# Performance work log

Measured on AMD Instinct MI355X. Metric: run time of the kernel, lower is better.

Reference implementation:

```python
import jax, jax.numpy as jnp
import numpy as np

DT = 0.01
NJ = 7  # panda: 7 revolute joints, serial chain, fixed base
G_ACC = 9.81


def skew(v):
    x, y, z = v[..., 0], v[..., 1], v[..., 2]
    O = jnp.zeros_like(x)
    return jnp.stack([jnp.stack([O, -z, y], -1),
                      jnp.stack([z, O, -x], -1),
                      jnp.stack([-y, x, O], -1)], -2)


def rodrigues(axis, q):
    # axis [3], q [B] -> [B,3,3]
    K = skew(axis)
    K2 = K @ K
    s = jnp.sin(q)[:, None, None]
    c = jnp.cos(q)[:, None, None]
    return jnp.eye(3, dtype=q.dtype) + s * K + (1.0 - c) * K2


def xmot(E, r, v):
    # motion transform child<-parent; E [B,3,3], r [3], v [B,6] ([w;u] ordering)
    w, u = v[:, :3], v[:, 3:]
    wn = jnp.einsum('bij,bj->bi', E, w)
    un = jnp.einsum('bij,bj->bi', E, u - jnp.cross(jnp.broadcast_to(r, u.shape), w))
    return jnp.concatenate([wn, un], -1)


def crm(v, m):
    # motion cross product v x m
    w, u = v[:, :3], v[:, 3:]
    return jnp.concatenate([jnp.cross(w, m[:, :3]),
                            jnp.cross(w, m[:, 3:]) + jnp.cross(u, m[:, :3])], -1)


def crf(v, f):
    # force cross product v x* f
    w, u = v[:, :3], v[:, 3:]
    n, ff = f[:, :3], f[:, 3:]
    return jnp.concatenate([jnp.cross(w, n) + jnp.cross(u, ff), jnp.cross(w, ff)], -1)


def spatial_inertia(mass, com, inertia):
    # [NJ] / [NJ,3] / [NJ,3,3] -> [NJ,6,6] in [w;v] ordering
    cx = skew(com)
    m = mass[:, None, None]
    top = jnp.concatenate([inertia + m * (cx @ jnp.swapaxes(cx, -1, -2)), m * cx], -1)
    bot = jnp.concatenate([m * jnp.swapaxes(cx, -1, -2),
                           m * jnp.broadcast_to(jnp.eye(3, dtype=mass.dtype), cx.shape)], -1)
    return jnp.concatenate([top, bot], -2)


def aba(q, qd, tau, axes, R_fix, p_fix, mass, com, inertia):
    B = q.shape[0]
    I6 = spatial_inertia(mass, com, inertia)  # [NJ,6,6]
    E_l, S_l, v_l, c_l, IA_l, pA_l = [], [], [], [], [], []
    v_prev = None
    # pass 1: kinematics + bias terms
    for i in range(NJ):
        Rw = jnp.einsum('ij,bjk->bik', R_fix[i], rodrigues(axes[i], q[:, i]))
        E = jnp.swapaxes(Rw, -1, -2)  # parent->child rotation
        S = jnp.concatenate([axes[i], jnp.zeros(3, dtype=q.dtype)])  # [6]
        vJ = qd[:, i:i + 1] * S
        v_i = vJ if i == 0 else xmot(E, p_fix[i], v_prev) + vJ
        c_i = crm(v_i, vJ)
        Iv = jnp.einsum('ij,bj->bi', I6[i], v_i)
        pA_i = crf(v_i, Iv)
        E_l.append(E); S_l.append(S); v_l.append(v_i); c_l.append(c_i)
        IA_l.append(jnp.broadcast_to(I6[i], (B, 6, 6)))
        pA_l.append(pA_i)
        v_prev = v_i
    # pass 2: articulated inertia backward sweep
    U_l = [None] * NJ; d_l = [None] * NJ; uu_l = [None] * NJ
    for i in reversed(range(NJ)):
        S = S_l[i]; IA = IA_l[i]
        U = jnp.einsum('bij,j->bi', IA, S)
        d = jnp.einsum('bi,i->b', U, S)
        uu = tau[:, i] - jnp.einsum('bi,i->b', pA_l[i], S)
        U_l[i], d_l[i], uu_l[i] = U, d, uu
        if i > 0:
            Ia = IA - U[:, :, None] * U[:, None, :] / d[:, None, None]
            pa = pA_l[i] + jnp.einsum('bij,bj->bi', Ia, c_l[i]) + U * (uu / d)[:, None]
            E = E_l[i]; rX = skew(p_fix[i])
            Z = jnp.zeros_like(E)
            Xm = jnp.concatenate([jnp.concatenate([E, Z], -1),
                                  jnp.concatenate([-jnp.einsum('bij,jk->bik', E, rX), E], -1)], -2)
            IA_l[i - 1] = IA_l[i - 1] + jnp.einsum('bji,bjk,bkl->bil', Xm, Ia, Xm)
            fE = jnp.einsum('bji,bj->bi', E, pa[:, 3:])
            nP = jnp.einsum('bji,bj->bi', E, pa[:, :3]) + jnp.cross(jnp.broadcast_to(p_fix[i], fE.shape), fE)
            pA_l[i - 1] = pA_l[i - 1] + jnp.concatenate([nP, fE], -1)
    # pass 3: accelerations (base spatial accel = -gravity)
    a_prev = jnp.broadcast_to(jnp.array([0, 0, 0, 0, 0, G_ACC], dtype=q.dtype), (B, 6))
    qdd = []
    for i in range(NJ):
        ap = xmot(E_l[i], p_fix[i], a_prev) + c_l[i]
        qdd_i = (uu_l[i] - jnp.einsum('bi,bi->b', U_l[i], ap)) / d_l[i]
        a_prev = ap + qdd_i[:, None] * S_l[i]
        qdd.append(qdd_i)
    return jnp.stack(qdd, -1)  # [B,NJ]


def _rx(a):
    c, s = np.cos(a), np.sin(a)
    return np.array([[1, 0, 0], [0, c, -s], [0, s, c]], np.float32)


def setup_inputs() -> dict:
    key = jax.random.key(0)
    k1, k2 = jax.random.split(key)
    B = 262144
    x = 0.5 * jax.random.normal(k1, (B, 2 * NJ), dtype=jnp.float32)
    u = 5.0 * jax.random.normal(k2, (B, NJ), dtype=jnp.float32)
    angles = [0.0, -np.pi / 2, np.pi / 2, np.pi / 2, -np.pi / 2, np.pi / 2, np.pi / 2]
    R_fix = jnp.asarray(np.stack([_rx(a) for a in angles]).astype(np.float32))
    p_fix = jnp.asarray(np.array([[0, 0, 0.333], [0, 0, 0], [0, -0.316, 0], [0.0825, 0, 0],
                                  [-0.0825, 0.384, 0], [0, 0, 0], [0.088, 0, 0]], np.float32))
    axes = jnp.asarray(np.tile(np.array([0, 0, 1], np.float32), (NJ, 1)))
    mass = jnp.asarray(np.array([4.97, 0.65, 3.23, 3.59, 1.23, 1.67, 0.735], np.float32))
    com = jnp.asarray(np.array([[0.003, 0.002, -0.06], [-0.003, -0.028, 0.003], [0.027, 0.039, -0.066],
                                [-0.053, 0.104, 0.027], [-0.012, 0.041, -0.038], [0.06, -0.014, -0.011],
                                [0.01, -0.004, 0.061]], np.float32))
    diags = np.array([[0.7, 0.7, 0.01], [0.008, 0.028, 0.025], [0.037, 0.036, 0.011],
                      [0.026, 0.028, 0.031], [0.036, 0.036, 0.011], [0.002, 0.004, 0.005],
                      [0.012, 0.010, 0.005]], np.float32)
    inertia = jnp.asarray(np.stack([np.diag(v) for v in diags]).astype(np.float32))
    return {"x": x, "u": u, "axes": axes, "R_fix": R_fix, "p_fix": p_fix,
            "mass": mass, "com": com, "inertia": inertia}


def reference(x, u, axes, R_fix, p_fix, mass, com, inertia):
    q, v = x[:, :NJ], x[:, NJ:]
    a = aba(q, v, u, axes, R_fix, p_fix, mass, com, inertia)
    v_next = v + DT * a            # semi-implicit Euler
    q_next = q + DT * v_next
    return jnp.concatenate([q_next, v_next], -1)
```

## Files before the change

kernel.cpp:

```cpp
#include <hip/hip_runtime.h>

#define NJ 7
#define TB 256
static constexpr float DT_C    = 0.01f;
static constexpr float G_ACC_C = 9.81f;

static constexpr float RF[NJ][9] = {
    {1,0,0,  0,1,0,  0,0,1},
    {1,0,0,  0,0,1,  0,-1,0},
    {1,0,0,  0,0,-1, 0,1,0},
    {1,0,0,  0,0,-1, 0,1,0},
    {1,0,0,  0,0,1,  0,-1,0},
    {1,0,0,  0,0,-1, 0,1,0},
    {1,0,0,  0,0,-1, 0,1,0},
};
static constexpr float PFX[NJ][3] = {
    {0.f, 0.f, 0.333f},
    {0.f, 0.f, 0.f},
    {0.f, -0.316f, 0.f},
    {0.0825f, 0.f, 0.f},
    {-0.0825f, 0.384f, 0.f},
    {0.f, 0.f, 0.f},
    {0.088f, 0.f, 0.f},
};
static constexpr float MS[NJ] = {4.97f, 0.65f, 3.23f, 3.59f, 1.23f, 1.67f, 0.735f};
static constexpr float CM[NJ][3] = {
    {0.003f, 0.002f, -0.06f},
    {-0.003f, -0.028f, 0.003f},
    {0.027f, 0.039f, -0.066f},
    {-0.053f, 0.104f, 0.027f},
    {-0.012f, 0.041f, -0.038f},
    {0.06f, -0.014f, -0.011f},
    {0.01f, -0.004f, 0.061f},
};
static constexpr float ID[NJ][3] = {
    {0.7f, 0.7f, 0.01f},
    {0.008f, 0.028f, 0.025f},
    {0.037f, 0.036f, 0.011f},
    {0.026f, 0.028f, 0.031f},
    {0.036f, 0.036f, 0.011f},
    {0.002f, 0.004f, 0.005f},
    {0.012f, 0.01f, 0.005f},
};

#define MAKE_E(Rf, s, c)                                                     \
    float E00 = (Rf)[0]*(c) + (Rf)[1]*(s);                                   \
    float E01 = (Rf)[3]*(c) + (Rf)[4]*(s);                                   \
    float E02 = (Rf)[6]*(c) + (Rf)[7]*(s);                                   \
    float E10 = (Rf)[1]*(c) - (Rf)[0]*(s);                                   \
    float E11 = (Rf)[4]*(c) - (Rf)[3]*(s);                                   \
    float E12 = (Rf)[7]*(c) - (Rf)[6]*(s);                                   \
    float E20 = (Rf)[2];                                                     \
    float E21 = (Rf)[5];                                                     \
    float E22 = (Rf)[8];

extern "C" __global__ __launch_bounds__(256)
void aba_step_kernel(const float* __restrict__ x, const float* __restrict__ u,
                     float* __restrict__ out, int B)
{
    __shared__ float xbuf [TB * 14];
    __shared__ float ubuf [TB * 7];
    __shared__ float scbuf[TB * 14];

    const int tid = threadIdx.x;
    const int b0  = blockIdx.x * TB;
    const int nb  = min(TB, B - b0);

    if (nb == TB) {
        const float4* xv = (const float4*)(x + b0 * 14);
        float4*       xl = (float4*)xbuf;
        #pragma unroll
        for (int k = 0; k < 4; ++k) {
            int idx = tid + k * TB;
            if (idx < 896) xl[idx] = xv[idx];
        }
        const float4* uv = (const float4*)(u + b0 * 7);
        float4*       ul = (float4*)ubuf;
        #pragma unroll
        for (int k = 0; k < 2; ++k) {
            int idx = tid + k * TB;
            if (idx < 448) ul[idx] = uv[idx];
        }
    } else {
        int nx = nb * 14;
        for (int t = tid; t < nx; t += TB) xbuf[t] = x[b0 * 14 + t];
        int nu = nb * 7;
        for (int t = tid; t < nu; t += TB) ubuf[t] = u[b0 * 7 + t];
    }
    __syncthreads();

    if (tid < nb) {
        const float* xr  = xbuf  + tid * 14;
        const float* ur  = ubuf  + tid * 7;
        float*       scr = scbuf + tid * 14;

        float cl0[NJ], cl1[NJ], cl3[NJ], cl4[NJ];
        float pA[NJ][6];

        {
            float v0=0.f, v1=0.f, v2=0.f, v3=0.f, v4=0.f, v5=0.f;
            #pragma unroll
            for (int i = 0; i < NJ; ++i) {
                float qi = xr[i];
                float qd = xr[7 + i];
                float s, c;
                __sincosf(qi, &s, &c);
                scr[i]     = s;
                scr[7 + i] = c;
                MAKE_E(RF[i], s, c)
                if (i == 0) {
                    v0 = 0.f; v1 = 0.f; v2 = qd; v3 = 0.f; v4 = 0.f; v5 = 0.f;
                } else {
                    const float px = PFX[i][0], py = PFX[i][1], pz = PFX[i][2];
                    float t0 = v3 - (py*v2 - pz*v1);
                    float t1 = v4 - (pz*v0 - px*v2);
                    float t2 = v5 - (px*v1 - py*v0);
                    float nw0 = E00*v0 + E01*v1 + E02*v2;
                    float nw1 = E10*v0 + E11*v1 + E12*v2;
                    float nw2 = E20*v0 + E21*v1 + E22*v2;
                    float nu0 = E00*t0 + E01*t1 + E02*t2;
                    float nu1 = E10*t0 + E11*t1 + E12*t2;
                    float nu2 = E20*t0 + E21*t1 + E22*t2;
                    v0 = nw0; v1 = nw1; v2 = nw2 + qd;
                    v3 = nu0; v4 = nu1; v5 = nu2;
                }
                cl0[i] =  v1*qd;
                cl1[i] = -v0*qd;
                cl3[i] =  v4*qd;
                cl4[i] = -v3*qd;
                const float m  = MS[i];
                const float cx = CM[i][0], cy = CM[i][1], cz = CM[i][2];
                const float cc = cx*cx + cy*cy + cz*cz;
                const float A0 = ID[i][0] + m*(cc - cx*cx);
                const float A1 = -(m*cx*cy);
                const float A2 = -(m*cx*cz);
                const float A3 = ID[i][1] + m*(cc - cy*cy);
                const float A4 = -(m*cy*cz);
                const float A5 = ID[i][2] + m*(cc - cz*cz);
                float n0 = A0*v0 + A1*v1 + A2*v2 + m*(cy*v5 - cz*v4);
                float n1 = A1*v0 + A3*v1 + A4*v2 + m*(cz*v3 - cx*v5);
                float n2 = A2*v0 + A4*v1 + A5*v2 + m*(cx*v4 - cy*v3);
                float f0 = m*(v1*cz - v2*cy + v3);
                float f1 = m*(v2*cx - v0*cz + v4);
                float f2 = m*(v0*cy - v1*cx + v5);
                pA[i][0] = v1*n2 - v2*n1 + v4*f2 - v5*f1;
                pA[i][1] = v2*n0 - v0*n2 + v5*f0 - v3*f2;
                pA[i][2] = v0*n1 - v1*n0 + v3*f1 - v4*f0;
                pA[i][3] = v1*f2 - v2*f1;
                pA[i][4] = v2*f0 - v0*f2;
                pA[i][5] = v0*f1 - v1*f0;
            }
        }

        float PA[6] = {0,0,0,0,0,0};
        float PB[9] = {0,0,0,0,0,0,0,0,0};
        float PC[6] = {0,0,0,0,0,0};

        #pragma unroll
        for (int ii = 0; ii < NJ; ++ii) {
            const int i = NJ - 1 - ii;
            const float m  = MS[i];
            const float cx = CM[i][0], cy = CM[i][1], cz = CM[i][2];
            const float cc = cx*cx + cy*cy + cz*cz;
            float A0 = ID[i][0] + m*(cc - cx*cx) + PA[0];
            float A1 = -(m*cx*cy)               + PA[1];
            float A2 = -(m*cx*cz)               + PA[2];
            float A3 = ID[i][1] + m*(cc - cy*cy) + PA[3];
            float A4 = -(m*cy*cz)               + PA[4];
            float A5 = ID[i][2] + m*(cc - cz*cz) + PA[5];
            float B00 = PB[0];          float B01 = PB[1] - m*cz;  float B02 = PB[2] + m*cy;
            float B10 = PB[3] + m*cz;   float B11 = PB[4];         float B12 = PB[5] - m*cx;
            float B20 = PB[6] - m*cy;   float B21 = PB[7] + m*cx;  float B22 = PB[8];
            float C0 = PC[0] + m, C1 = PC[1],     C2 = PC[2];
            float C3 = PC[3] + m, C4 = PC[4],     C5 = PC[5] + m;

            float uu   = ur[i] - pA[i][2];
            float invd = __builtin_amdgcn_rcpf(A5);
            float k    = uu * invd;
            float t0 = A2*invd, t1 = A4*invd;
            float t3 = B20*invd, t4 = B21*invd, t5 = B22*invd;

            if (i > 0) {
                float a00 = A0 - A2*t0, a01 = A1 - A2*t1, a11 = A3 - A4*t1;
                float b00 = B00 - A2*t3, b01 = B01 - A2*t4, b02 = B02 - A2*t5;
                float b10 = B10 - A4*t3, b11 = B11 - A4*t4, b12 = B12 - A4*t5;
                float c00 = C0 - B20*t3, c01 = C1 - B20*t4, c02 = C2 - B20*t5;
                float c11 = C3 - B21*t4, c12 = C4 - B21*t5, c22 = C5 - B22*t5;

                float q0 = cl0[i], q1 = cl1[i], q3 = cl3[i], q4 = cl4[i];
                float pa0 = pA[i][0] + a00*q0 + a01*q1 + b00*q3 + b01*q4 + A2*k;
                float pa1 = pA[i][1] + a01*q0 + a11*q1 + b10*q3 + b11*q4 + A4*k;
                float pa2 = pA[i][2] + uu;
                float pa3 = pA[i][3] + b00*q0 + b10*q1 + c00*q3 + c01*q4 + B20*k;
                float pa4 = pA[i][4] + b01*q0 + b11*q1 + c01*q3 + c11*q4 + B21*k;
                float pa5 = pA[i][5] + b02*q0 + b12*q1 + c02*q3 + c12*q4 + B22*k;

                float s = scr[i], c = scr[7 + i];
                MAKE_E(RF[i], s, c)
                const float px = PFX[i][0], py = PFX[i][1], pz = PFX[i][2];

                float AE00 = a00*E00 + a01*E10, AE01 = a00*E01 + a01*E11, AE02 = a00*E02 + a01*E12;
                float AE10 = a01*E00 + a11*E10, AE11 = a01*E01 + a11*E11, AE12 = a01*E02 + a11*E12;
                float Ap00 = E00*AE00 + E10*AE10;
                float Ap01 = E00*AE01 + E10*AE11;
                float Ap02 = E00*AE02 + E10*AE12;
                float Ap11 = E01*AE01 + E11*AE11;
                float Ap12 = E01*AE02 + E11*AE12;
                float Ap22 = E02*AE02 + E12*AE12;
                float BE00 = b00*E00 + b01*E10 + b02*E20;
                float BE01 = b00*E01 + b01*E11 + b02*E21;
                float BE02 = b00*E02 + b01*E12 + b02*E22;
                float BE10 = b10*E00 + b11*E10 + b12*E20;
                float BE11 = b10*E01 + b11*E11 + b12*E21;
                float BE12 = b10*E02 + b11*E12 + b12*E22;
                float Bp00 = E00*BE00 + E10*BE10, Bp01 = E00*BE01 + E10*BE11, Bp02 = E00*BE02 + E10*BE12;
                float Bp10 = E01*BE00 + E11*BE10, Bp11 = E01*BE01 + E11*BE11, Bp12 = E01*BE02 + E11*BE12;
                float Bp20 = E02*BE00 + E12*BE10, Bp21 = E02*BE01 + E12*BE11, Bp22 = E02*BE02 + E12*BE12;
                float CE00 = c00*E00 + c01*E10 + c02*E20;
                float CE01 = c00*E01 + c01*E11 + c02*E21;
                float CE02 = c00*E02 + c01*E12 + c02*E22;
                float CE10 = c01*E00 + c11*E10 + c12*E20;
                float CE11 = c01*E01 + c11*E11 + c12*E21;
                float CE12 = c01*E02 + c11*E12 + c12*E22;
                float CE20 = c02*E00 + c12*E10 + c22*E20;
                float CE21 = c02*E01 + c12*E11 + c22*E21;
                float CE22 = c02*E02 + c12*E12 + c22*E22;
                float Cp00 = E00*CE00 + E10*CE10 + E20*CE20;
                float Cp01 = E00*CE01 + E10*CE11 + E20*CE21;
                float Cp02 = E00*CE02 + E10*CE12 + E20*CE22;
                float Cp11 = E01*CE01 + E11*CE11 + E21*CE21;
                float Cp12 = E01*CE02 + E11*CE12 + E21*CE22;
                float Cp22 = E02*CE02 + E12*CE12 + E22*CE22;
                float G00 = Bp01*pz - Bp02*py, G01 = Bp02*px - Bp00*pz, G02 = Bp00*py - Bp01*px;
                float G10 = Bp11*pz - Bp12*py, G11 = Bp12*px - Bp10*pz, G12 = Bp10*py - Bp11*px;
                float G20 = Bp21*pz - Bp22*py, G21 = Bp22*px - Bp20*pz, G22 = Bp20*py - Bp21*px;
                float H00 = Cp01*pz - Cp02*py, H01 = Cp02*px - Cp00*pz, H02 = Cp00*py - Cp01*px;
                float H10 = Cp11*pz - Cp12*py, H11 = Cp12*px - Cp01*pz, H12 = Cp01*py - Cp11*px;
                float H20 = Cp12*pz - Cp22*py, H21 = Cp22*px - Cp02*pz, H22 = Cp02*py - Cp12*px;
                float PH00 = py*H20 - pz*H10;
                float PH01 = py*H21 - pz*H11;
                float PH02 = py*H22 - pz*H12;
                float PH11 = pz*H01 - px*H21;
                float PH12 = pz*H02 - px*H22;
                float PH22 = px*H12 - py*H02;
                PA[0] = Ap00 - G00 - G00 - PH00;
                PA[1] = Ap01 - G01 - G10 - PH01;
                PA[2] = Ap02 - G02 - G20 - PH02;
                PA[3] = Ap11 - G11 - G11 - PH11;
                PA[4] = Ap12 - G12 - G21 - PH12;
                PA[5] = Ap22 - G22 - G22 - PH22;
                PB[0] = Bp00 + py*Cp02 - pz*Cp01;
                PB[1] = Bp01 + py*Cp12 - pz*Cp11;
                PB[2] = Bp02 + py*Cp22 - pz*Cp12;
                PB[3] = Bp10 + pz*Cp00 - px*Cp02;
                PB[4] = Bp11 + pz*Cp01 - px*Cp12;
                PB[5] = Bp12 + pz*Cp02 - px*Cp22;
                PB[6] = Bp20 + px*Cp01 - py*Cp00;
                PB[7] = Bp21 + px*Cp11 - py*Cp01;
                PB[8] = Bp22 + px*Cp12 - py*Cp02;
                PC[0] = Cp00; PC[1] = Cp01; PC[2] = Cp02;
                PC[3] = Cp11; PC[4] = Cp12; PC[5] = Cp22;
                float fE0 = E00*pa3 + E10*pa4 + E20*pa5;
                float fE1 = E01*pa3 + E11*pa4 + E21*pa5;
                float fE2 = E02*pa3 + E12*pa4 + E22*pa5;
                float nP0 = E00*pa0 + E10*pa1 + E20*pa2 + (py*fE2 - pz*fE1);
                float nP1 = E01*pa0 + E11*pa1 + E21*pa2 + (pz*fE0 - px*fE2);
                float nP2 = E02*pa0 + E12*pa1 + E22*pa2 + (px*fE1 - py*fE0);
                pA[i-1][0] += nP0; pA[i-1][1] += nP1; pA[i-1][2] += nP2;
                pA[i-1][3] += fE0; pA[i-1][4] += fE1; pA[i-1][5] += fE2;
            }
            pA[i][0] = t0; pA[i][1] = t1; pA[i][2] = t3;
            pA[i][3] = t4; pA[i][4] = t5; pA[i][5] = k;
        }

        {
            float a0=0.f, a1=0.f, a2=0.f, a3=0.f, a4=0.f, a5=G_ACC_C;
            #pragma unroll
            for (int i = 0; i < NJ; ++i) {
                float qi = xr[i];
                float qd = xr[7 + i];
                float s = scr[i], c = scr[7 + i];
                MAKE_E(RF[i], s, c)
                const float px = PFX[i][0], py = PFX[i][1], pz = PFX[i][2];
                float t0 = a3 - (py*a2 - pz*a1);
                float t1 = a4 - (pz*a0 - px*a2);
                float t2 = a5 - (px*a1 - py*a0);
                float ap0 = E00*a0 + E01*a1 + E02*a2 + cl0[i];
                float ap1 = E10*a0 + E11*a1 + E12*a2 + cl1[i];
                float ap2 = E20*a0 + E21*a1 + E22*a2;
                float ap3 = E00*t0 + E01*t1 + E02*t2 + cl3[i];
                float ap4 = E10*t0 + E11*t1 + E12*t2 + cl4[i];
                float ap5 = E20*t0 + E21*t1 + E22*t2;
                float qdd = pA[i][5] - (pA[i][0]*ap0 + pA[i][1]*ap1 + ap2
                                      + pA[i][2]*ap3 + pA[i][3]*ap4 + pA[i][4]*ap5);
                a0 = ap0; a1 = ap1; a2 = ap2 + qdd;
                a3 = ap3; a4 = ap4; a5 = ap5;
                float vn = qd + DT_C*qdd;
                scr[7 + i] = vn;
                scr[i]     = qi + DT_C*vn;
            }
        }
    }

    __syncthreads();
    if (nb == TB) {
        float4*       ov = (float4*)(out + b0 * 14);
        const float4* sl = (const float4*)scbuf;
        #pragma unroll
        for (int k = 0; k < 4; ++k) {
            int idx = tid + k * TB;
            if (idx < 896) ov[idx] = sl[idx];
        }
    } else {
        int nx = nb * 14;
        for (int t = tid; t < nx; t += TB) out[b0 * 14 + t] = scbuf[t];
    }
}

extern "C" void kernel_launch(void* const* d_in, const int* in_sizes, int n_in,
                              void* d_out, int out_size, void* d_ws, size_t ws_size,
                              hipStream_t stream) {
    const float* x = (const float*)d_in[0];
    const float* u = (const float*)d_in[1];
    float* out = (float*)d_out;
    int B = in_sizes[0] / (2*NJ);
    int threads = TB;
    int blocks = (B + threads - 1) / threads;
    hipLaunchKernelGGL(aba_step_kernel, dim3(blocks), dim3(threads), 0, stream,
                       x, u, out, B);
}
```

Measured before the change: 105.9 us.

## Recompute bias forces and velocities to cut registers and shared memory

Pass 1 now keeps only the per-link spatial velocities. Bias forces, Coriolis terms and sincos are recomputed later in the backward and forward passes instead of being held in register arrays or a shared-memory scratch buffer. The forward pass reruns the velocity recursion and writes results in place into the input buffer, removing the separate scratch LDS array. The launch bounds request 4 blocks per CU, trading extra arithmetic for lower register and LDS pressure and higher occupancy.

```diff
diff --git a/kernel.cpp b/kernel.cpp
--- a/kernel.cpp
+++ b/kernel.cpp
@@ -54,13 +54,12 @@
     float E21 = (Rf)[5];                                                     \
     float E22 = (Rf)[8];
 
-extern "C" __global__ __launch_bounds__(256)
+extern "C" __global__ __launch_bounds__(256, 4)
 void aba_step_kernel(const float* __restrict__ x, const float* __restrict__ u,
                      float* __restrict__ out, int B)
 {
     __shared__ float xbuf [TB * 14];
     __shared__ float ubuf [TB * 7];
-    __shared__ float scbuf[TB * 14];
 
     const int tid = threadIdx.x;
     const int b0  = blockIdx.x * TB;
@@ -90,27 +89,23 @@
     __syncthreads();
 
     if (tid < nb) {
-        const float* xr  = xbuf  + tid * 14;
-        const float* ur  = ubuf  + tid * 7;
-        float*       scr = scbuf + tid * 14;
-
-        float cl0[NJ], cl1[NJ], cl3[NJ], cl4[NJ];
-        float pA[NJ][6];
+        const float* xr = xbuf + tid * 14;
+        const float* ur = ubuf + tid * 7;
+        float*       xw = xbuf + tid * 14;
+
+        float V[NJ][6];
 
         {
             float v0=0.f, v1=0.f, v2=0.f, v3=0.f, v4=0.f, v5=0.f;
             #pragma unroll
             for (int i = 0; i < NJ; ++i) {
-                float qi = xr[i];
-                float qd = xr[7 + i];
-                float s, c;
-                __sincosf(qi, &s, &c);
-                scr[i]     = s;
-                scr[7 + i] = c;
-                MAKE_E(RF[i], s, c)
+                const float qd = xr[7 + i];
                 if (i == 0) {
-                    v0 = 0.f; v1 = 0.f; v2 = qd; v3 = 0.f; v4 = 0.f; v5 = 0.f;
+                    v2 = qd;
                 } else {
+                    float s, c;
+                    __sincosf(xr[i], &s, &c);
+                    MAKE_E(RF[i], s, c)
                     const float px = PFX[i][0], py = PFX[i][1], pz = PFX[i][2];
                     float t0 = v3 - (py*v2 - pz*v1);
                     float t1 = v4 - (pz*v0 - px*v2);
@@ -124,57 +119,55 @@
                     v0 = nw0; v1 = nw1; v2 = nw2 + qd;
                     v3 = nu0; v4 = nu1; v5 = nu2;
                 }
-                cl0[i] =  v1*qd;
-                cl1[i] = -v0*qd;
-                cl3[i] =  v4*qd;
-                cl4[i] = -v3*qd;
-                const float m  = MS[i];
-                const float cx = CM[i][0], cy = CM[i][1], cz = CM[i][2];
-                const float cc = cx*cx + cy*cy + cz*cz;
-                const float A0 = ID[i][0] + m*(cc - cx*cx);
-                const float A1 = -(m*cx*cy);
-                const float A2 = -(m*cx*cz);
-                const float A3 = ID[i][1] + m*(cc - cy*cy);
-                const float A4 = -(m*cy*cz);
-                const float A5 = ID[i][2] + m*(cc - cz*cz);
-                float n0 = A0*v0 + A1*v1 + A2*v2 + m*(cy*v5 - cz*v4);
-                float n1 = A1*v0 + A3*v1 + A4*v2 + m*(cz*v3 - cx*v5);
-                float n2 = A2*v0 + A4*v1 + A5*v2 + m*(cx*v4 - cy*v3);
-                float f0 = m*(v1*cz - v2*cy + v3);
-                float f1 = m*(v2*cx - v0*cz + v4);
-                float f2 = m*(v0*cy - v1*cx + v5);
-                pA[i][0] = v1*n2 - v2*n1 + v4*f2 - v5*f1;
-                pA[i][1] = v2*n0 - v0*n2 + v5*f0 - v3*f2;
-                pA[i][2] = v0*n1 - v1*n0 + v3*f1 - v4*f0;
-                pA[i][3] = v1*f2 - v2*f1;
-                pA[i][4] = v2*f0 - v0*f2;
-                pA[i][5] = v0*f1 - v1*f0;
+                V[i][0]=v0; V[i][1]=v1; V[i][2]=v2;
+                V[i][3]=v3; V[i][4]=v4; V[i][5]=v5;
             }
         }
 
         float PA[6] = {0,0,0,0,0,0};
         float PB[9] = {0,0,0,0,0,0,0,0,0};
         float PC[6] = {0,0,0,0,0,0};
+        float AC0=0.f, AC1=0.f, AC2=0.f, AC3=0.f, AC4=0.f, AC5=0.f;
 
         #pragma unroll
         for (int ii = 0; ii < NJ; ++ii) {
             const int i = NJ - 1 - ii;
+            const float qd = xr[7 + i];
+            const float v0 = V[i][0], v1 = V[i][1], v2 = V[i][2];
+            const float v3 = V[i][3], v4 = V[i][4], v5 = V[i][5];
+
             const float m  = MS[i];
             const float cx = CM[i][0], cy = CM[i][1], cz = CM[i][2];
             const float cc = cx*cx + cy*cy + cz*cz;
-            float A0 = ID[i][0] + m*(cc - cx*cx) + PA[0];
-            float A1 = -(m*cx*cy)               + PA[1];
-            float A2 = -(m*cx*cz)               + PA[2];
-            float A3 = ID[i][1] + m*(cc - cy*cy) + PA[3];
-            float A4 = -(m*cy*cz)               + PA[4];
-            float A5 = ID[i][2] + m*(cc - cz*cz) + PA[5];
+            const float J0 = ID[i][0] + m*(cc - cx*cx);
+            const float J1 = -(m*cx*cy);
+            const float J2 = -(m*cx*cz);
+            const float J3 = ID[i][1] + m*(cc - cy*cy);
+            const float J4 = -(m*cy*cz);
+            const float J5 = ID[i][2] + m*(cc - cz*cz);
+
+            float n0 = J0*v0 + J1*v1 + J2*v2 + m*(cy*v5 - cz*v4);
+            float n1 = J1*v0 + J3*v1 + J4*v2 + m*(cz*v3 - cx*v5);
+            float n2 = J2*v0 + J4*v1 + J5*v2 + m*(cx*v4 - cy*v3);
+            float f0 = m*(v1*cz - v2*cy + v3);
+            float f1 = m*(v2*cx - v0*cz + v4);
+            float f2 = m*(v0*cy - v1*cx + v5);
+            float p0 = v1*n2 - v2*n1 + v4*f2 - v5*f1 + AC0;
+            float p1 = v2*n0 - v0*n2 + v5*f0 - v3*f2 + AC1;
+            float p2 = v0*n1 - v1*n0 + v3*f1 - v4*f0 + AC2;
+            float p3 = v1*f2 - v2*f1 + AC3;
+            float p4 = v2*f0 - v0*f2 + AC4;
+            float p5 = v0*f1 - v1*f0 + AC5;
+
+            float A0 = J0 + PA[0]; float A1 = J1 + PA[1]; float A2 = J2 + PA[2];
+            float A3 = J3 + PA[3]; float A4 = J4 + PA[4]; float A5 = J5 + PA[5];
             float B00 = PB[0];          float B01 = PB[1] - m*cz;  float B02 = PB[2] + m*cy;
             float B10 = PB[3] + m*cz;   float B11 = PB[4];         float B12 = PB[5] - m*cx;
             float B20 = PB[6] - m*cy;   float B21 = PB[7] + m*cx;  float B22 = PB[8];
             float C0 = PC[0] + m, C1 = PC[1],     C2 = PC[2];
             float C3 = PC[3] + m, C4 = PC[4],     C5 = PC[5] + m;
 
-            float uu   = ur[i] - pA[i][2];
+            float uu   = ur[i] - p2;
             float invd = __builtin_amdgcn_rcpf(A5);
             float k    = uu * invd;
             float t0 = A2*invd, t1 = A4*invd;
@@ -187,17 +180,26 @@
                 float c00 = C0 - B20*t3, c01 = C1 - B20*t4, c02 = C2 - B20*t5;
                 float c11 = C3 - B21*t4, c12 = C4 - B21*t5, c22 = C5 - B22*t5;
 
-                float q0 = cl0[i], q1 = cl1[i], q3 = cl3[i], q4 = cl4[i];
-                float pa0 = pA[i][0] + a00*q0 + a01*q1 + b00*q3 + b01*q4 + A2*k;
-                float pa1 = pA[i][1] + a01*q0 + a11*q1 + b10*q3 + b11*q4 + A4*k;
-                float pa2 = pA[i][2] + uu;
-                float pa3 = pA[i][3] + b00*q0 + b10*q1 + c00*q3 + c01*q4 + B20*k;
-                float pa4 = pA[i][4] + b01*q0 + b11*q1 + c01*q3 + c11*q4 + B21*k;
-                float pa5 = pA[i][5] + b02*q0 + b12*q1 + c02*q3 + c12*q4 + B22*k;
-
-                float s = scr[i], c = scr[7 + i];
+                float q0 = v1*qd, q1 = -v0*qd, q3 = v4*qd, q4 = -v3*qd;
+                float pa0 = p0 + a00*q0 + a01*q1 + b00*q3 + b01*q4 + A2*k;
+                float pa1 = p1 + a01*q0 + a11*q1 + b10*q3 + b11*q4 + A4*k;
+                float pa2 = p2 + uu;
+                float pa3 = p3 + b00*q0 + b10*q1 + c00*q3 + c01*q4 + B20*k;
+                float pa4 = p4 + b01*q0 + b11*q1 + c01*q3 + c11*q4 + B21*k;
+                float pa5 = p5 + b02*q0 + b12*q1 + c02*q3 + c12*q4 + B22*k;
+
+                float s, c;
+                __sincosf(xr[i], &s, &c);
                 MAKE_E(RF[i], s, c)
                 const float px = PFX[i][0], py = PFX[i][1], pz = PFX[i][2];
+
+                float fE0 = E00*pa3 + E10*pa4 + E20*pa5;
+                float fE1 = E01*pa3 + E11*pa4 + E21*pa5;
+                float fE2 = E02*pa3 + E12*pa4 + E22*pa5;
+                AC0 = E00*pa0 + E10*pa1 + E20*pa2 + (py*fE2 - pz*fE1);
+                AC1 = E01*pa0 + E11*pa1 + E21*pa2 + (pz*fE0 - px*fE2);
+                AC2 = E02*pa0 + E12*pa1 + E22*pa2 + (px*fE1 - py*fE0);
+                AC3 = fE0; AC4 = fE1; AC5 = fE2;
 
                 float AE00 = a00*E00 + a01*E10, AE01 = a00*E01 + a01*E11, AE02 = a00*E02 + a01*E12;
                 float AE10 = a01*E00 + a11*E10, AE11 = a01*E01 + a11*E11, AE12 = a01*E02 + a11*E12;
@@ -260,44 +262,53 @@
                 PB[8] = Bp22 + px*Cp12 - py*Cp02;
                 PC[0] = Cp00; PC[1] = Cp01; PC[2] = Cp02;
                 PC[3] = Cp11; PC[4] = Cp12; PC[5] = Cp22;
-                float fE0 = E00*pa3 + E10*pa4 + E20*pa5;
-                float fE1 = E01*pa3 + E11*pa4 + E21*pa5;
-                float fE2 = E02*pa3 + E12*pa4 + E22*pa5;
-                float nP0 = E00*pa0 + E10*pa1 + E20*pa2 + (py*fE2 - pz*fE1);
-                float nP1 = E01*pa0 + E11*pa1 + E21*pa2 + (pz*fE0 - px*fE2);
-                float nP2 = E02*pa0 + E12*pa1 + E22*pa2 + (px*fE1 - py*fE0);
-                pA[i-1][0] += nP0; pA[i-1][1] += nP1; pA[i-1][2] += nP2;
-                pA[i-1][3] += fE0; pA[i-1][4] += fE1; pA[i-1][5] += fE2;
             }
-            pA[i][0] = t0; pA[i][1] = t1; pA[i][2] = t3;
-            pA[i][3] = t4; pA[i][4] = t5; pA[i][5] = k;
+            V[i][0]=t0; V[i][1]=t1; V[i][2]=t3; V[i][3]=t4; V[i][4]=t5; V[i][5]=k;
         }
 
         {
             float a0=0.f, a1=0.f, a2=0.f, a3=0.f, a4=0.f, a5=G_ACC_C;
+            float w0=0.f, w1=0.f, w2=0.f, w3=0.f, w4=0.f, w5=0.f;
             #pragma unroll
             for (int i = 0; i < NJ; ++i) {
-                float qi = xr[i];
-                float qd = xr[7 + i];
-                float s = scr[i], c = scr[7 + i];
+                const float qi = xr[i];
+                const float qd = xr[7 + i];
+                float s, c;
+                __sincosf(qi, &s, &c);
                 MAKE_E(RF[i], s, c)
                 const float px = PFX[i][0], py = PFX[i][1], pz = PFX[i][2];
-                float t0 = a3 - (py*a2 - pz*a1);
-                float t1 = a4 - (pz*a0 - px*a2);
-                float t2 = a5 - (px*a1 - py*a0);
-                float ap0 = E00*a0 + E01*a1 + E02*a2 + cl0[i];
-                float ap1 = E10*a0 + E11*a1 + E12*a2 + cl1[i];
+                if (i == 0) {
+                    w0=0.f; w1=0.f; w2=qd; w3=0.f; w4=0.f; w5=0.f;
+                } else {
+                    float r0 = w3 - (py*w2 - pz*w1);
+                    float r1 = w4 - (pz*w0 - px*w2);
+                    float r2 = w5 - (px*w1 - py*w0);
+                    float nw0 = E00*w0 + E01*w1 + E02*w2;
+                    float nw1 = E10*w0 + E11*w1 + E12*w2;
+                    float nw2 = E20*w0 + E21*w1 + E22*w2;
+                    float nu0 = E00*r0 + E01*r1 + E02*r2;
+                    float nu1 = E10*r0 + E11*r1 + E12*r2;
+                    float nu2 = E20*r0 + E21*r1 + E22*r2;
+                    w0 = nw0; w1 = nw1; w2 = nw2 + qd;
+                    w3 = nu0; w4 = nu1; w5 = nu2;
+                }
+                float cl0 = w1*qd, cl1 = -w0*qd, cl3 = w4*qd, cl4 = -w3*qd;
+                float r0 = a3 - (py*a2 - pz*a1);
+                float r1 = a4 - (pz*a0 - px*a2);
+                float r2 = a5 - (px*a1 - py*a0);
+                float ap0 = E00*a0 + E01*a1 + E02*a2 + cl0;
+                float ap1 = E10*a0 + E11*a1 + E12*a2 + cl1;
                 float ap2 = E20*a0 + E21*a1 + E22*a2;
-                float ap3 = E00*t0 + E01*t1 + E02*t2 + cl3[i];
-                float ap4 = E10*t0 + E11*t1 + E12*t2 + cl4[i];
-                float ap5 = E20*t0 + E21*t1 + E22*t2;
-                float qdd = pA[i][5] - (pA[i][0]*ap0 + pA[i][1]*ap1 + ap2
-                                      + pA[i][2]*ap3 + pA[i][3]*ap4 + pA[i][4]*ap5);
+                float ap3 = E00*r0 + E01*r1 + E02*r2 + cl3;
+                float ap4 = E10*r0 + E11*r1 + E12*r2 + cl4;
+                float ap5 = E20*r0 + E21*r1 + E22*r2;
+                float qdd = V[i][5] - (V[i][0]*ap0 + V[i][1]*ap1 + ap2
+                                     + V[i][2]*ap3 + V[i][3]*ap4 + V[i][4]*ap5);
                 a0 = ap0; a1 = ap1; a2 = ap2 + qdd;
                 a3 = ap3; a4 = ap4; a5 = ap5;
                 float vn = qd + DT_C*qdd;
-                scr[7 + i] = vn;
-                scr[i]     = qi + DT_C*vn;
+                xw[7 + i] = vn;
+                xw[i]     = qi + DT_C*vn;
             }
         }
     }
@@ -305,7 +316,7 @@
     __syncthreads();
     if (nb == TB) {
         float4*       ov = (float4*)(out + b0 * 14);
-        const float4* sl = (const float4*)scbuf;
+        const float4* sl = (const float4*)xbuf;
         #pragma unroll
         for (int k = 0; k < 4; ++k) {
             int idx = tid + k * TB;
@@ -313,7 +324,7 @@
         }
     } else {
         int nx = nb * 14;
-        for (int t = tid; t < nx; t += TB) out[b0 * 14 + t] = scbuf[t];
+        for (int t = tid; t < nx; t += TB) out[b0 * 14 + t] = xbuf[t];
     }
 }
 
```

Result: slower. 139.9 us (+32.1%).
